# Performance work log

Hardware: AMD Instinct MI355X
Metric: run time of the kernel (lower is better)

The kernel has to match this reference:

```python
import jax, jax.numpy as jnp
import numpy as np

B, S, D = 8, 512, 1024
F = 4 * D        # FFN hidden
E = 8            # num experts
SCALE = 0.02


def setup_inputs() -> dict:
    key = jax.random.key(0)
    ks = jax.random.split(key, 16)
    n = lambda k, shape, s=SCALE: (jax.random.normal(k, shape, dtype=jnp.float32) * s)
    task_ids = jax.random.randint(ks[15], (B,), 0, E)
    return {
        "hidden_states": jax.random.normal(ks[0], (B, S, D), dtype=jnp.float32),
        "ohe_task": jax.nn.one_hot(task_ids, E, dtype=jnp.float32),
        # base model (2-layer FFN) params
        "W1": n(ks[1], (D, F)), "b1": n(ks[2], (F,)),
        "W2": n(ks[3], (F, D)), "b2": n(ks[4], (D,)),
        # expert task vectors (expert_sd - base_sd), stacked over experts
        "T_W1": n(ks[5], (E, D, F)), "T_b1": n(ks[6], (E, F)),
        "T_W2": n(ks[7], (E, F, D)), "T_b2": n(ks[8], (E, D)),
        # gate: 2 hidden ReLU layers then linear to E
        "Wg1": n(ks[9], (D, D)), "bg1": jnp.zeros((D,), jnp.float32),
        "Wg2": n(ks[10], (D, D)), "bg2": jnp.zeros((D,), jnp.float32),
        "Wgo": n(ks[11], (D, E)), "bgo": jnp.zeros((E,), jnp.float32),
    }


def reference(hidden_states, ohe_task, W1, b1, W2, b2,
              T_W1, T_b1, T_W2, T_b2,
              Wg1, bg1, Wg2, bg2, Wgo, bgo):
    x = hidden_states  # [B,S,D]
    # --- router: per-token logits -> softmax over experts -> mean over seq ---
    h = jax.nn.relu(jnp.einsum("bsd,de->bse", x, Wg1) + bg1)
    h = jax.nn.relu(jnp.einsum("bsd,de->bse", h, Wg2) + bg2)
    logits = jnp.einsum("bsd,de->bse", h, Wgo) + bgo        # [B,S,E]
    gate_weights = jax.nn.softmax(logits, axis=-1).mean(axis=1)  # [B,E]
    # --- per-sample weighted merge of expert task vectors into base params ---
    coeff = gate_weights + ohe_task                          # [B,E]
    W1b = W1 + jnp.einsum("be,edf->bdf", coeff, T_W1)        # [B,D,F]
    b1b = b1 + coeff @ T_b1                                  # [B,F]
    W2b = W2 + jnp.einsum("be,efd->bfd", coeff, T_W2)        # [B,F,D]
    b2b = b2 + coeff @ T_b2                                  # [B,D]
    # --- batched functional forward through merged FFN ---
    hmid = jax.nn.gelu(jnp.einsum("bsd,bdf->bsf", x, W1b) + b1b[:, None, :],
                       approximate=False)
    out = jnp.einsum("bsf,bfd->bsd", hmid, W2b) + b2b[:, None, :]
    return out, gate_weights
```

## Files before the change

### kernel.cpp

```cpp
#include <hip/hip_runtime.h>
#include <hip/hip_bf16.h>

typedef __attribute__((ext_vector_type(8))) short s16x8;
typedef __attribute__((ext_vector_type(4))) float f32x4;

#define GLOAD_LDS16(gsrc, ldst) \
  __builtin_amdgcn_global_load_lds((const __attribute__((address_space(1))) void*)(gsrc), \
      (__attribute__((address_space(3))) void*)(ldst), 16, 0, 0)

__global__ __launch_bounds__(256) void cvt_bf16(const float* __restrict__ in,
                                                __hip_bfloat16* __restrict__ out, long n) {
  long i = ((long)blockIdx.x * 256 + threadIdx.x) * 4;
  if (i + 3 >= n) return;
  float4 v = *(const float4*)(in + i);
  __hip_bfloat16 tmp[4] = {__float2bfloat16(v.x), __float2bfloat16(v.y),
                           __float2bfloat16(v.z), __float2bfloat16(v.w)};
  *(ushort4*)((unsigned short*)out + i) = *(const ushort4*)tmp;
}

template<int NB>
__global__ __launch_bounds__(256) void merge_transpose(
    const float* __restrict__ Wb, const float* __restrict__ T,
    const float* __restrict__ coeff, __hip_bfloat16* __restrict__ Out,
    int K, int N, int nE) {
  int ntn = N >> 6;
  int k0 = (blockIdx.x / ntn) << 6;
  int n0 = (blockIdx.x % ntn) << 6;
  int t = threadIdx.x;
  long KN = (long)K * N;

  float4 accb[NB][4];
#pragma unroll
  for (int i = 0; i < 4; ++i) {
    int e = i * 256 + t; int kk = e >> 4, nn = (e & 15) << 2;
    float4 bv = *(const float4*)&Wb[(long)(k0 + kk) * N + n0 + nn];
#pragma unroll
    for (int b2 = 0; b2 < NB; ++b2) accb[b2][i] = bv;
  }
  for (int ex = 0; ex < nE; ++ex) {
    float c[NB];
#pragma unroll
    for (int b2 = 0; b2 < NB; ++b2) c[b2] = coeff[b2 * 8 + ex];
#pragma unroll
    for (int i = 0; i < 4; ++i) {
      int e = i * 256 + t; int kk = e >> 4, nn = (e & 15) << 2;
      float4 tv = *(const float4*)&T[(long)ex * KN + (long)(k0 + kk) * N + n0 + nn];
#pragma unroll
      for (int b2 = 0; b2 < NB; ++b2) {
        accb[b2][i].x += c[b2] * tv.x; accb[b2][i].y += c[b2] * tv.y;
        accb[b2][i].z += c[b2] * tv.z; accb[b2][i].w += c[b2] * tv.w;
      }
    }
  }
  __shared__ __hip_bfloat16 lds[64 * 66];
  for (int b2 = 0; b2 < NB; ++b2) {
    __syncthreads();
#pragma unroll
    for (int i = 0; i < 4; ++i) {
      int e = i * 256 + t; int kk = e >> 4, nn = (e & 15) << 2;
      lds[kk * 66 + nn + 0] = __float2bfloat16(accb[b2][i].x);
      lds[kk * 66 + nn + 1] = __float2bfloat16(accb[b2][i].y);
      lds[kk * 66 + nn + 2] = __float2bfloat16(accb[b2][i].z);
      lds[kk * 66 + nn + 3] = __float2bfloat16(accb[b2][i].w);
    }
    __syncthreads();
#pragma unroll
    for (int i = 0; i < 4; ++i) {
      int o = i * 256 + t; int n2 = o >> 4, k2 = (o & 15) << 2;
      __hip_bfloat16 tmp[4];
#pragma unroll
      for (int j = 0; j < 4; ++j) tmp[j] = lds[(k2 + j) * 66 + n2];
      *(ushort4*)((unsigned short*)&Out[(long)b2 * KN + (long)(n0 + n2) * K + k0 + k2]) =
          *(const ushort4*)tmp;
    }
  }
}

__global__ __launch_bounds__(256) void merge_bias(const float* __restrict__ base,
                                                  const float* __restrict__ T,
                                                  const float* __restrict__ coeff,
                                                  float* __restrict__ out, int n) {
  int b = blockIdx.y;
  int i = blockIdx.x * 256 + threadIdx.x;
  if (i >= n) return;
  float v = base[i];
#pragma unroll
  for (int e = 0; e < 8; ++e) v += coeff[b * 8 + e] * T[(long)e * n + i];
  out[(long)b * n + i] = v;
}

template<int ACT, bool OUTBF>
__global__ __launch_bounds__(256, 2) void gemm_bt(
    const __hip_bfloat16* __restrict__ A, const __hip_bfloat16* __restrict__ BT,
    const float* __restrict__ bias, void* __restrict__ Out,
    int M, int N, int K, long sA, long sB, long sBias, long sOut) {
  int b = blockIdx.y;
  const __hip_bfloat16* Ab = A + (long)b * sA;
  const __hip_bfloat16* Bb = BT + (long)b * sB;
  const float* biasb = bias + (long)b * sBias;

  int ntn = N >> 7;
  int m0 = (blockIdx.x / ntn) << 7;
  int n0 = (blockIdx.x % ntn) << 7;

  __shared__ __align__(16) __hip_bfloat16 As[2][128 * 64];
  __shared__ __align__(16) __hip_bfloat16 Bs[2][128 * 64];

  int t = threadIdx.x;
  int lane = t & 63;
  int wid = t >> 6;
  int wm = wid >> 1, wn = wid & 1;
  int lr = lane & 15, kg = lane >> 4;

  f32x4 acc[4][4] = {};

  auto stage = [&](int buf, int ktile) {
    int kt = ktile << 6;
#pragma unroll
    for (int is = 0; is < 4; ++is) {
      int ci = is * 256 + t;
      int row = ci >> 3, cpos = ci & 7;
      int csrc = cpos ^ (row & 7);
      GLOAD_LDS16(Ab + (long)(m0 + row) * K + kt + csrc * 8, &As[buf][ci * 8]);
      GLOAD_LDS16(Bb + (long)(n0 + row) * K + kt + csrc * 8, &Bs[buf][ci * 8]);
    }
  };

  auto compute = [&](int buf) {
#pragma unroll
    for (int ks = 0; ks < 2; ++ks) {
      s16x8 af[4], bfr[4];
#pragma unroll
      for (int m = 0; m < 4; ++m) {
        int row = wm * 64 + m * 16 + lr;
        int c = (ks * 4 + kg) ^ (row & 7);
        af[m] = *(const s16x8*)&As[buf][row * 64 + c * 8];
      }
#pragma unroll
      for (int n = 0; n < 4; ++n) {
        int row = wn * 64 + n * 16 + lr;
        int c = (ks * 4 + kg) ^ (row & 7);
        bfr[n] = *(const s16x8*)&Bs[buf][row * 64 + c * 8];
      }
#pragma unroll
      for (int m = 0; m < 4; ++m)
#pragma unroll
        for (int n = 0; n < 4; ++n)
          acc[m][n] = __builtin_amdgcn_mfma_f32_16x16x32_bf16(af[m], bfr[n], acc[m][n], 0, 0, 0);
    }
  };

  int nk = K >> 6;
  stage(0, 0);
  __syncthreads();
  for (int it = 0; it < nk - 1; ++it) {
    stage((it + 1) & 1, it + 1);
    compute(it & 1);
    __syncthreads();
  }
  compute((nk - 1) & 1);

#pragma unroll
  for (int n = 0; n < 4; ++n) {
    int col = n0 + wn * 64 + n * 16 + lr;
    float bv = biasb[col];
#pragma unroll
    for (int m = 0; m < 4; ++m) {
      int row0 = m0 + wm * 64 + m * 16 + kg * 4;
#pragma unroll
      for (int j = 0; j < 4; ++j) {
        float v = acc[m][n][j] + bv;
        if (ACT == 1) v = fmaxf(v, 0.f);
        else if (ACT == 2) v = 0.5f * v * (1.f + erff(v * 0.70710678118f));
        long off = (long)b * sOut + (long)(row0 + j) * N + col;
        if (OUTBF) ((__hip_bfloat16*)Out)[off] = __float2bfloat16(v);
        else ((float*)Out)[off] = v;
      }
    }
  }
}

__global__ __launch_bounds__(256) void router_logits(
    const __hip_bfloat16* __restrict__ Hg2, const float* __restrict__ Wgo,
    const float* __restrict__ bgo, float* __restrict__ probs) {
  int r = blockIdx.x;
  int t = threadIdx.x;
  float acc[8] = {};
#pragma unroll
  for (int j = 0; j < 4; ++j) {
    int k = j * 256 + t;
    float h = __bfloat162float(Hg2[(long)r * 1024 + k]);
    const float4* wp = (const float4*)&Wgo[k * 8];
    float4 w0 = wp[0], w1 = wp[1];
    acc[0] += h * w0.x; acc[1] += h * w0.y; acc[2] += h * w0.z; acc[3] += h * w0.w;
    acc[4] += h * w1.x; acc[5] += h * w1.y; acc[6] += h * w1.z; acc[7] += h * w1.w;
  }
#pragma unroll
  for (int off = 32; off >= 1; off >>= 1)
#pragma unroll
    for (int e = 0; e < 8; ++e) acc[e] += __shfl_down(acc[e], off);
  __shared__ float lds[4][8];
  int wid = t >> 6, lane = t & 63;
  if (lane == 0)
#pragma unroll
    for (int e = 0; e < 8; ++e) lds[wid][e] = acc[e];
  __syncthreads();
  if (t == 0) {
    float lg[8];
#pragma unroll
    for (int e = 0; e < 8; ++e) lg[e] = lds[0][e] + lds[1][e] + lds[2][e] + lds[3][e] + bgo[e];
    float mx = lg[0];
#pragma unroll
    for (int e = 1; e < 8; ++e) mx = fmaxf(mx, lg[e]);
    float s = 0.f;
#pragma unroll
    for (int e = 0; e < 8; ++e) { lg[e] = __expf(lg[e] - mx); s += lg[e]; }
    float inv = 1.f / s;
#pragma unroll
    for (int e = 0; e < 8; ++e) probs[(long)r * 8 + e] = lg[e] * inv;
  }
}

__global__ __launch_bounds__(256) void router_mean(
    const float* __restrict__ probs, const float* __restrict__ ohe,
    float* __restrict__ gate_out, float* __restrict__ coeff) {
  int b = blockIdx.x;
  int t = threadIdx.x;
  int e = t & 7, sg = t >> 3;
  float s = 0.f;
#pragma unroll
  for (int j = 0; j < 16; ++j)
    s += probs[((long)b * 512 + sg + j * 32) * 8 + e];
  __shared__ float lds[256];
  lds[t] = s;
  __syncthreads();
  if (t < 8) {
    float tot = 0.f;
#pragma unroll
    for (int g = 0; g < 32; ++g) tot += lds[g * 8 + t];
    float gw = tot / 512.f;
    gate_out[b * 8 + t] = gw;
    coeff[b * 8 + t] = gw + ohe[b * 8 + t];
  }
}

extern "C" void kernel_launch(void* const* d_in, const int* in_sizes, int n_in,
                              void* d_out, int out_size, void* d_ws, size_t ws_size,
                              hipStream_t stream) {
  const float* x    = (const float*)d_in[0];
  const float* ohe  = (const float*)d_in[1];
  const float* W1   = (const float*)d_in[2];
  const float* b1   = (const float*)d_in[3];
  const float* W2   = (const float*)d_in[4];
  const float* b2   = (const float*)d_in[5];
  const float* T_W1 = (const float*)d_in[6];
  const float* T_b1 = (const float*)d_in[7];
  const float* T_W2 = (const float*)d_in[8];
  const float* T_b2 = (const float*)d_in[9];
  const float* Wg1  = (const float*)d_in[10];
  const float* bg1  = (const float*)d_in[11];
  const float* Wg2  = (const float*)d_in[12];
  const float* bg2  = (const float*)d_in[13];
  const float* Wgo  = (const float*)d_in[14];
  const float* bgo  = (const float*)d_in[15];
  float* out = (float*)d_out;
  float* gate_out = out + (long)8 * 512 * 1024;

  char* w = (char*)d_ws;
  __hip_bfloat16* xb   = (__hip_bfloat16*)(w);
  __hip_bfloat16* Wg1T = (__hip_bfloat16*)(w + 8388608);
  __hip_bfloat16* Wg2T = (__hip_bfloat16*)(w + 10485760);
  __hip_bfloat16* Hg1  = (__hip_bfloat16*)(w + 12582912);
  __hip_bfloat16* Hg2  = (__hip_bfloat16*)(w + 20971520);
  float*          probs= (float*)(w + 29360128);
  float*          coeff= (float*)(w + 29491200);
  float*          b1b  = (float*)(w + 29492224);
  float*          b2b  = (float*)(w + 29623296);
  __hip_bfloat16* hmid = (__hip_bfloat16*)(w + 29656064);
  __hip_bfloat16* Wb   = (__hip_bfloat16*)(w + 63210496);

  cvt_bf16<<<4096, 256, 0, stream>>>(x, xb, (long)8 * 512 * 1024);
  merge_transpose<1><<<16 * 16, 256, 0, stream>>>(Wg1, nullptr, nullptr, Wg1T, 1024, 1024, 0);
  merge_transpose<1><<<16 * 16, 256, 0, stream>>>(Wg2, nullptr, nullptr, Wg2T, 1024, 1024, 0);
  gemm_bt<1, true><<<dim3(32 * 8, 1), 256, 0, stream>>>(xb, Wg1T, bg1, Hg1,
      4096, 1024, 1024, 0, 0, 0, 0);
  gemm_bt<1, true><<<dim3(32 * 8, 1), 256, 0, stream>>>(Hg1, Wg2T, bg2, Hg2,
      4096, 1024, 1024, 0, 0, 0, 0);
  router_logits<<<4096, 256, 0, stream>>>(Hg2, Wgo, bgo, probs);
  router_mean<<<8, 256, 0, stream>>>(probs, ohe, gate_out, coeff);
  merge_bias<<<dim3(16, 8), 256, 0, stream>>>(b1, T_b1, coeff, b1b, 4096);
  merge_bias<<<dim3(4, 8), 256, 0, stream>>>(b2, T_b2, coeff, b2b, 1024);
  merge_transpose<8><<<16 * 64, 256, 0, stream>>>(W1, T_W1, coeff, Wb, 1024, 4096, 8);
  gemm_bt<2, true><<<dim3(4 * 32, 8), 256, 0, stream>>>(xb, Wb, b1b, hmid,
      512, 4096, 1024, (long)512 * 1024, (long)4096 * 1024, 4096, (long)512 * 4096);
  merge_transpose<8><<<64 * 16, 256, 0, stream>>>(W2, T_W2, coeff, Wb, 4096, 1024, 8);
  gemm_bt<0, false><<<dim3(4 * 8, 8), 256, 0, stream>>>(hmid, Wb, b2b, out,
      512, 1024, 4096, (long)512 * 4096, (long)4096 * 1024, 1024, (long)512 * 1024);
}
```

Baseline: 288.9 us.

## Use 256-row tiles for FFN GEMMs with split-K second GEMM and reduction

```diff
diff --git a/kernel.cpp b/kernel.cpp
--- a/kernel.cpp
+++ b/kernel.cpp
@@ -103,8 +103,8 @@
   int m0 = (blockIdx.x / ntn) << 7;
   int n0 = (blockIdx.x % ntn) << 7;
 
-  __shared__ __align__(16) __hip_bfloat16 As[2][128 * 64];
-  __shared__ __align__(16) __hip_bfloat16 Bs[2][128 * 64];
+  __shared__ __align__(16) __hip_bfloat16 As[128 * 64];
+  __shared__ __align__(16) __hip_bfloat16 Bs[128 * 64];
 
   int t = threadIdx.x;
   int lane = t & 63;
@@ -114,19 +114,16 @@
 
   f32x4 acc[4][4] = {};
 
-  auto stage = [&](int buf, int ktile) {
-    int kt = ktile << 6;
+  for (int kt = 0; kt < K; kt += 64) {
 #pragma unroll
     for (int is = 0; is < 4; ++is) {
       int ci = is * 256 + t;
       int row = ci >> 3, cpos = ci & 7;
       int csrc = cpos ^ (row & 7);
-      GLOAD_LDS16(Ab + (long)(m0 + row) * K + kt + csrc * 8, &As[buf][ci * 8]);
-      GLOAD_LDS16(Bb + (long)(n0 + row) * K + kt + csrc * 8, &Bs[buf][ci * 8]);
-    }
-  };
-
-  auto compute = [&](int buf) {
+      GLOAD_LDS16(Ab + (long)(m0 + row) * K + kt + csrc * 8, &As[ci * 8]);
+      GLOAD_LDS16(Bb + (long)(n0 + row) * K + kt + csrc * 8, &Bs[ci * 8]);
+    }
+    __syncthreads();
 #pragma unroll
     for (int ks = 0; ks < 2; ++ks) {
       s16x8 af[4], bfr[4];
@@ -134,13 +131,13 @@
       for (int m = 0; m < 4; ++m) {
         int row = wm * 64 + m * 16 + lr;
         int c = (ks * 4 + kg) ^ (row & 7);
-        af[m] = *(const s16x8*)&As[buf][row * 64 + c * 8];
+        af[m] = *(const s16x8*)&As[row * 64 + c * 8];
       }
 #pragma unroll
       for (int n = 0; n < 4; ++n) {
         int row = wn * 64 + n * 16 + lr;
         int c = (ks * 4 + kg) ^ (row & 7);
-        bfr[n] = *(const s16x8*)&Bs[buf][row * 64 + c * 8];
+        bfr[n] = *(const s16x8*)&Bs[row * 64 + c * 8];
       }
 #pragma unroll
       for (int m = 0; m < 4; ++m)
@@ -148,17 +145,8 @@
         for (int n = 0; n < 4; ++n)
           acc[m][n] = __builtin_amdgcn_mfma_f32_16x16x32_bf16(af[m], bfr[n], acc[m][n], 0, 0, 0);
     }
-  };
-
-  int nk = K >> 6;
-  stage(0, 0);
-  __syncthreads();
-  for (int it = 0; it < nk - 1; ++it) {
-    stage((it + 1) & 1, it + 1);
-    compute(it & 1);
     __syncthreads();
   }
-  compute((nk - 1) & 1);
 
 #pragma unroll
   for (int n = 0; n < 4; ++n) {
@@ -178,6 +166,132 @@
       }
     }
   }
+}
+
+template<int BN, int ACT, bool OUTBF>
+__global__ __launch_bounds__(512, 2) void gemm256(
+    const __hip_bfloat16* __restrict__ A, const __hip_bfloat16* __restrict__ BT,
+    const float* __restrict__ bias, void* __restrict__ Out,
+    int M, int N, int K, long sA, long sB, long sBias, long sOut,
+    int kLen, int nmn, long ksOut) {
+  constexpr int NR = BN / 64;
+  constexpr int BLOADS = (BN * 64 * 2) / (512 * 16);
+  int b = blockIdx.y;
+  int kc = blockIdx.x / nmn;
+  int rest = blockIdx.x % nmn;
+  int ntn = N / BN;
+  int m0 = (rest / ntn) << 8;
+  int n0 = (rest % ntn) * BN;
+  int kOff = kc * kLen;
+  const __hip_bfloat16* Ab = A + (long)b * sA;
+  const __hip_bfloat16* Bb = BT + (long)b * sB;
+
+  __shared__ __align__(16) __hip_bfloat16 As[2][256 * 64];
+  __shared__ __align__(16) __hip_bfloat16 Bs[2][BN * 64];
+
+  int t = threadIdx.x;
+  int lane = t & 63;
+  int wid = t >> 6;
+  int wm = wid >> 2;
+  int wn = wid & 3;
+  int lr = lane & 15, kg = lane >> 4;
+
+  f32x4 acc[8][NR] = {};
+
+  auto stage = [&](int buf, int kt) {
+#pragma unroll
+    for (int is = 0; is < 4; ++is) {
+      int ci = is * 512 + t;
+      int row = ci >> 3, cpos = ci & 7;
+      int csrc = cpos ^ (row & 7);
+      GLOAD_LDS16(Ab + (long)(m0 + row) * K + kt + csrc * 8, &As[buf][ci * 8]);
+    }
+#pragma unroll
+    for (int is = 0; is < BLOADS; ++is) {
+      int ci = is * 512 + t;
+      int row = ci >> 3, cpos = ci & 7;
+      int csrc = cpos ^ (row & 7);
+      GLOAD_LDS16(Bb + (long)(n0 + row) * K + kt + csrc * 8, &Bs[buf][ci * 8]);
+    }
+  };
+
+  auto compute = [&](int buf) {
+#pragma unroll
+    for (int ks = 0; ks < 2; ++ks) {
+      s16x8 af[8], bfr[NR];
+#pragma unroll
+      for (int m = 0; m < 8; ++m) {
+        int row = wm * 128 + m * 16 + lr;
+        int c = (ks * 4 + kg) ^ (row & 7);
+        af[m] = *(const s16x8*)&As[buf][row * 64 + c * 8];
+      }
+#pragma unroll
+      for (int n = 0; n < NR; ++n) {
+        int row = wn * (BN / 4) + n * 16 + lr;
+        int c = (ks * 4 + kg) ^ (row & 7);
+        bfr[n] = *(const s16x8*)&Bs[buf][row * 64 + c * 8];
+      }
+#pragma unroll
+      for (int m = 0; m < 8; ++m)
+#pragma unroll
+        for (int n = 0; n < NR; ++n)
+          acc[m][n] = __builtin_amdgcn_mfma_f32_16x16x32_bf16(af[m], bfr[n], acc[m][n], 0, 0, 0);
+    }
+  };
+
+  int nk = kLen >> 6;
+  stage(0, kOff);
+  __syncthreads();
+  for (int it = 0; it < nk - 1; ++it) {
+    stage((it + 1) & 1, kOff + ((it + 1) << 6));
+    compute(it & 1);
+    __syncthreads();
+  }
+  compute((nk - 1) & 1);
+
+  char* outb = (char*)Out;
+#pragma unroll
+  for (int n = 0; n < NR; ++n) {
+    int col = n0 + wn * (BN / 4) + n * 16 + lr;
+    float bv = (bias != nullptr) ? bias[(long)b * sBias + col] : 0.f;
+#pragma unroll
+    for (int m = 0; m < 8; ++m) {
+      int row0 = m0 + wm * 128 + m * 16 + kg * 4;
+#pragma unroll
+      for (int j = 0; j < 4; ++j) {
+        float v = acc[m][n][j] + bv;
+        if (ACT == 1) v = fmaxf(v, 0.f);
+        else if (ACT == 2) v = 0.5f * v * (1.f + erff(v * 0.70710678118f));
+        long off = kc * ksOut + (long)b * sOut + (long)(row0 + j) * N + col;
+        if (OUTBF) ((__hip_bfloat16*)outb)[off] = __float2bfloat16(v);
+        else ((float*)outb)[off] = v;
+      }
+    }
+  }
+}
+
+__global__ __launch_bounds__(256) void reduce2_bias(
+    const __hip_bfloat16* __restrict__ p, const float* __restrict__ b2b,
+    float* __restrict__ out, long ksOut) {
+  long i = ((long)blockIdx.x * 256 + threadIdx.x) * 8;
+  const unsigned short* ps = (const unsigned short*)p;
+  ushort4 a0 = *(const ushort4*)(ps + i);
+  ushort4 a1 = *(const ushort4*)(ps + i + 4);
+  ushort4 c0 = *(const ushort4*)(ps + ksOut + i);
+  ushort4 c1 = *(const ushort4*)(ps + ksOut + i + 4);
+  int d = (int)(i & 1023);
+  int b = (int)(i >> 19);
+  const float* bp = b2b + (long)b * 1024 + d;
+  float o[8];
+  unsigned short av[8] = {a0.x, a0.y, a0.z, a0.w, a1.x, a1.y, a1.z, a1.w};
+  unsigned short cv[8] = {c0.x, c0.y, c0.z, c0.w, c1.x, c1.y, c1.z, c1.w};
+#pragma unroll
+  for (int j = 0; j < 8; ++j) {
+    __hip_bfloat16 ab = *(__hip_bfloat16*)&av[j], cb = *(__hip_bfloat16*)&cv[j];
+    o[j] = __bfloat162float(ab) + __bfloat162float(cb) + bp[j];
+  }
+  *(float4*)(out + i) = make_float4(o[0], o[1], o[2], o[3]);
+  *(float4*)(out + i + 4) = make_float4(o[4], o[5], o[6], o[7]);
 }
 
 __global__ __launch_bounds__(256) void router_logits(
@@ -278,6 +392,10 @@
   float*          b2b  = (float*)(w + 29623296);
   __hip_bfloat16* hmid = (__hip_bfloat16*)(w + 29656064);
   __hip_bfloat16* Wb   = (__hip_bfloat16*)(w + 63210496);
+  __hip_bfloat16* part = (__hip_bfloat16*)(w);
+
+  const long SSD = (long)512 * 1024;
+  const long SSF = (long)512 * 4096;
 
   cvt_bf16<<<4096, 256, 0, stream>>>(x, xb, (long)8 * 512 * 1024);
   merge_transpose<1><<<16 * 16, 256, 0, stream>>>(Wg1, nullptr, nullptr, Wg1T, 1024, 1024, 0);
@@ -291,9 +409,10 @@
   merge_bias<<<dim3(16, 8), 256, 0, stream>>>(b1, T_b1, coeff, b1b, 4096);
   merge_bias<<<dim3(4, 8), 256, 0, stream>>>(b2, T_b2, coeff, b2b, 1024);
   merge_transpose<8><<<16 * 64, 256, 0, stream>>>(W1, T_W1, coeff, Wb, 1024, 4096, 8);
-  gemm_bt<2, true><<<dim3(4 * 32, 8), 256, 0, stream>>>(xb, Wb, b1b, hmid,
-      512, 4096, 1024, (long)512 * 1024, (long)4096 * 1024, 4096, (long)512 * 4096);
+  gemm256<256, 2, true><<<dim3(2 * 16, 8), 512, 0, stream>>>(xb, Wb, b1b, hmid,
+      512, 4096, 1024, SSD, (long)4096 * 1024, 4096, SSF, 1024, 2 * 16, 0);
   merge_transpose<8><<<64 * 16, 256, 0, stream>>>(W2, T_W2, coeff, Wb, 4096, 1024, 8);
-  gemm_bt<0, false><<<dim3(4 * 8, 8), 256, 0, stream>>>(hmid, Wb, b2b, out,
-      512, 1024, 4096, (long)512 * 4096, (long)4096 * 1024, 1024, (long)512 * 1024);
-}
+  gemm256<128, 0, true><<<dim3(2 * 8 * 2, 8), 512, 0, stream>>>(hmid, Wb, nullptr, part,
+      512, 1024, 4096, SSF, (long)4096 * 1024, 0, SSD, 2048, 2 * 8, (long)8 * 512 * 1024);
+  reduce2_bias<<<2048, 256, 0, stream>>>(part, b2b, out, (long)8 * 512 * 1024);
+}
```

Result: slower. 325.4 us (+12.6%).

## Split-K final GEMM with XCD-aware tile mapping and single-buffered LDS

Applied to the files above, without the earlier changes.

```diff
diff --git a/kernel.cpp b/kernel.cpp
--- a/kernel.cpp
+++ b/kernel.cpp
@@ -89,22 +89,27 @@
   out[(long)b * n + i] = v;
 }
 
-template<int ACT, bool OUTBF>
+template<int MODE, int ACT, bool OUTBF>
 __global__ __launch_bounds__(256, 2) void gemm_bt(
     const __hip_bfloat16* __restrict__ A, const __hip_bfloat16* __restrict__ BT,
     const float* __restrict__ bias, void* __restrict__ Out,
-    int M, int N, int K, long sA, long sB, long sBias, long sOut) {
+    int N, int K, long sA, long sB, long sBias, long sOut,
+    int kLen, long ksOut) {
   int b = blockIdx.y;
+  int bid = blockIdx.x;
+  int slot = bid & 7, inner = bid >> 3;
+  int m, n, kc = 0;
+  if (MODE == 0)      { m = slot * 4 + (inner & 3); n = inner >> 2; }
+  else if (MODE == 1) { m = slot >> 1; n = ((slot & 1) << 4) | inner; }
+  else                { m = slot >> 1; kc = slot & 1; n = inner; }
+  int m0 = m << 7, n0 = n << 7;
+  int kOff = kc * kLen;
+
   const __hip_bfloat16* Ab = A + (long)b * sA;
   const __hip_bfloat16* Bb = BT + (long)b * sB;
-  const float* biasb = bias + (long)b * sBias;
-
-  int ntn = N >> 7;
-  int m0 = (blockIdx.x / ntn) << 7;
-  int n0 = (blockIdx.x % ntn) << 7;
-
-  __shared__ __align__(16) __hip_bfloat16 As[2][128 * 64];
-  __shared__ __align__(16) __hip_bfloat16 Bs[2][128 * 64];
+
+  __shared__ __align__(16) __hip_bfloat16 As[128 * 64];
+  __shared__ __align__(16) __hip_bfloat16 Bs[128 * 64];
 
   int t = threadIdx.x;
   int lane = t & 63;
@@ -114,70 +119,92 @@
 
   f32x4 acc[4][4] = {};
 
-  auto stage = [&](int buf, int ktile) {
-    int kt = ktile << 6;
+  for (int kt = kOff; kt < kOff + kLen; kt += 64) {
 #pragma unroll
     for (int is = 0; is < 4; ++is) {
       int ci = is * 256 + t;
       int row = ci >> 3, cpos = ci & 7;
       int csrc = cpos ^ (row & 7);
-      GLOAD_LDS16(Ab + (long)(m0 + row) * K + kt + csrc * 8, &As[buf][ci * 8]);
-      GLOAD_LDS16(Bb + (long)(n0 + row) * K + kt + csrc * 8, &Bs[buf][ci * 8]);
-    }
-  };
-
-  auto compute = [&](int buf) {
+      GLOAD_LDS16(Ab + (long)(m0 + row) * K + kt + csrc * 8, &As[ci * 8]);
+      GLOAD_LDS16(Bb + (long)(n0 + row) * K + kt + csrc * 8, &Bs[ci * 8]);
+    }
+    __syncthreads();
 #pragma unroll
     for (int ks = 0; ks < 2; ++ks) {
       s16x8 af[4], bfr[4];
 #pragma unroll
-      for (int m = 0; m < 4; ++m) {
-        int row = wm * 64 + m * 16 + lr;
+      for (int mi = 0; mi < 4; ++mi) {
+        int row = wm * 64 + mi * 16 + lr;
         int c = (ks * 4 + kg) ^ (row & 7);
-        af[m] = *(const s16x8*)&As[buf][row * 64 + c * 8];
-      }
-#pragma unroll
-      for (int n = 0; n < 4; ++n) {
-        int row = wn * 64 + n * 16 + lr;
+        af[mi] = *(const s16x8*)&As[row * 64 + c * 8];
+      }
+#pragma unroll
+      for (int ni = 0; ni < 4; ++ni) {
+        int row = wn * 64 + ni * 16 + lr;
         int c = (ks * 4 + kg) ^ (row & 7);
-        bfr[n] = *(const s16x8*)&Bs[buf][row * 64 + c * 8];
-      }
-#pragma unroll
-      for (int m = 0; m < 4; ++m)
-#pragma unroll
-        for (int n = 0; n < 4; ++n)
-          acc[m][n] = __builtin_amdgcn_mfma_f32_16x16x32_bf16(af[m], bfr[n], acc[m][n], 0, 0, 0);
-    }
-  };
-
-  int nk = K >> 6;
-  stage(0, 0);
-  __syncthreads();
-  for (int it = 0; it < nk - 1; ++it) {
-    stage((it + 1) & 1, it + 1);
-    compute(it & 1);
+        bfr[ni] = *(const s16x8*)&Bs[row * 64 + c * 8];
+      }
+#pragma unroll
+      for (int mi = 0; mi < 4; ++mi)
+#pragma unroll
+        for (int ni = 0; ni < 4; ++ni)
+          acc[mi][ni] = __builtin_amdgcn_mfma_f32_16x16x32_bf16(bfr[ni], af[mi], acc[mi][ni], 0, 0, 0);
+    }
     __syncthreads();
   }
-  compute((nk - 1) & 1);
-
-#pragma unroll
-  for (int n = 0; n < 4; ++n) {
-    int col = n0 + wn * 64 + n * 16 + lr;
-    float bv = biasb[col];
-#pragma unroll
-    for (int m = 0; m < 4; ++m) {
-      int row0 = m0 + wm * 64 + m * 16 + kg * 4;
+
+#pragma unroll
+  for (int mi = 0; mi < 4; ++mi) {
+    int row = m0 + wm * 64 + mi * 16 + lr;
+#pragma unroll
+    for (int ni = 0; ni < 4; ++ni) {
+      int colb = n0 + wn * 64 + ni * 16 + kg * 4;
+      float bv4[4] = {0.f, 0.f, 0.f, 0.f};
+      if (bias != nullptr) {
+        float4 bb = *(const float4*)&bias[(long)b * sBias + colb];
+        bv4[0] = bb.x; bv4[1] = bb.y; bv4[2] = bb.z; bv4[3] = bb.w;
+      }
+      float v[4];
 #pragma unroll
       for (int j = 0; j < 4; ++j) {
-        float v = acc[m][n][j] + bv;
-        if (ACT == 1) v = fmaxf(v, 0.f);
-        else if (ACT == 2) v = 0.5f * v * (1.f + erff(v * 0.70710678118f));
-        long off = (long)b * sOut + (long)(row0 + j) * N + col;
-        if (OUTBF) ((__hip_bfloat16*)Out)[off] = __float2bfloat16(v);
-        else ((float*)Out)[off] = v;
-      }
-    }
-  }
+        v[j] = acc[mi][ni][j] + bv4[j];
+        if (ACT == 1) v[j] = fmaxf(v[j], 0.f);
+        else if (ACT == 2) v[j] = 0.5f * v[j] * (1.f + erff(v[j] * 0.70710678118f));
+      }
+      long off = kc * ksOut + (long)b * sOut + (long)row * N + colb;
+      if (OUTBF) {
+        __hip_bfloat16 tmp[4] = {__float2bfloat16(v[0]), __float2bfloat16(v[1]),
+                                 __float2bfloat16(v[2]), __float2bfloat16(v[3])};
+        *(ushort4*)((unsigned short*)Out + off) = *(const ushort4*)tmp;
+      } else {
+        *(float4*)((float*)Out + off) = make_float4(v[0], v[1], v[2], v[3]);
+      }
+    }
+  }
+}
+
+__global__ __launch_bounds__(256) void reduce2_bias(
+    const __hip_bfloat16* __restrict__ p, const float* __restrict__ b2b,
+    float* __restrict__ out, long ksOut) {
+  long i = ((long)blockIdx.x * 256 + threadIdx.x) * 8;
+  const unsigned short* ps = (const unsigned short*)p;
+  ushort4 a0 = *(const ushort4*)(ps + i);
+  ushort4 a1 = *(const ushort4*)(ps + i + 4);
+  ushort4 c0 = *(const ushort4*)(ps + ksOut + i);
+  ushort4 c1 = *(const ushort4*)(ps + ksOut + i + 4);
+  int d = (int)(i & 1023);
+  int b = (int)(i >> 19);
+  const float* bp = b2b + (long)b * 1024 + d;
+  float o[8];
+  unsigned short av[8] = {a0.x, a0.y, a0.z, a0.w, a1.x, a1.y, a1.z, a1.w};
+  unsigned short cv[8] = {c0.x, c0.y, c0.z, c0.w, c1.x, c1.y, c1.z, c1.w};
+#pragma unroll
+  for (int j = 0; j < 8; ++j) {
+    __hip_bfloat16 ab = *(__hip_bfloat16*)&av[j], cb = *(__hip_bfloat16*)&cv[j];
+    o[j] = __bfloat162float(ab) + __bfloat162float(cb) + bp[j];
+  }
+  *(float4*)(out + i) = make_float4(o[0], o[1], o[2], o[3]);
+  *(float4*)(out + i + 4) = make_float4(o[4], o[5], o[6], o[7]);
 }
 
 __global__ __launch_bounds__(256) void router_logits(
@@ -278,22 +305,27 @@
   float*          b2b  = (float*)(w + 29623296);
   __hip_bfloat16* hmid = (__hip_bfloat16*)(w + 29656064);
   __hip_bfloat16* Wb   = (__hip_bfloat16*)(w + 63210496);
+  __hip_bfloat16* part = (__hip_bfloat16*)(w);
+
+  const long SSD = (long)512 * 1024;
+  const long SSF = (long)512 * 4096;
 
   cvt_bf16<<<4096, 256, 0, stream>>>(x, xb, (long)8 * 512 * 1024);
   merge_transpose<1><<<16 * 16, 256, 0, stream>>>(Wg1, nullptr, nullptr, Wg1T, 1024, 1024, 0);
   merge_transpose<1><<<16 * 16, 256, 0, stream>>>(Wg2, nullptr, nullptr, Wg2T, 1024, 1024, 0);
-  gemm_bt<1, true><<<dim3(32 * 8, 1), 256, 0, stream>>>(xb, Wg1T, bg1, Hg1,
-      4096, 1024, 1024, 0, 0, 0, 0);
-  gemm_bt<1, true><<<dim3(32 * 8, 1), 256, 0, stream>>>(Hg1, Wg2T, bg2, Hg2,
-      4096, 1024, 1024, 0, 0, 0, 0);
+  gemm_bt<0, 1, true><<<dim3(256, 1), 256, 0, stream>>>(xb, Wg1T, bg1, Hg1,
+      1024, 1024, 0, 0, 0, 0, 1024, 0);
+  gemm_bt<0, 1, true><<<dim3(256, 1), 256, 0, stream>>>(Hg1, Wg2T, bg2, Hg2,
+      1024, 1024, 0, 0, 0, 0, 1024, 0);
   router_logits<<<4096, 256, 0, stream>>>(Hg2, Wgo, bgo, probs);
   router_mean<<<8, 256, 0, stream>>>(probs, ohe, gate_out, coeff);
   merge_bias<<<dim3(16, 8), 256, 0, stream>>>(b1, T_b1, coeff, b1b, 4096);
   merge_bias<<<dim3(4, 8), 256, 0, stream>>>(b2, T_b2, coeff, b2b, 1024);
   merge_transpose<8><<<16 * 64, 256, 0, stream>>>(W1, T_W1, coeff, Wb, 1024, 4096, 8);
-  gemm_bt<2, true><<<dim3(4 * 32, 8), 256, 0, stream>>>(xb, Wb, b1b, hmid,
-      512, 4096, 1024, (long)512 * 1024, (long)4096 * 1024, 4096, (long)512 * 4096);
+  gemm_bt<1, 2, true><<<dim3(128, 8), 256, 0, stream>>>(xb, Wb, b1b, hmid,
+      4096, 1024, SSD, (long)4096 * 1024, 4096, SSF, 1024, 0);
   merge_transpose<8><<<64 * 16, 256, 0, stream>>>(W2, T_W2, coeff, Wb, 4096, 1024, 8);
-  gemm_bt<0, false><<<dim3(4 * 8, 8), 256, 0, stream>>>(hmid, Wb, b2b, out,
-      512, 1024, 4096, (long)512 * 4096, (long)4096 * 1024, 1024, (long)512 * 1024);
-}
+  gemm_bt<2, 0, true><<<dim3(64, 8), 256, 0, stream>>>(hmid, Wb, nullptr, part,
+      1024, 4096, SSF, (long)4096 * 1024, 0, SSD, 2048, (long)8 * 512 * 1024);
+  reduce2_bias<<<2048, 256, 0, stream>>>(part, b2b, out, (long)8 * 512 * 1024);
+}
```

After: 275.2 us. 1.05x faster.
